# Kernel tuning notes

Hardware: AMD Instinct MI355X
Metric: run time of the kernel (lower is better)

Reference implementation:

```python
import jax, jax.numpy as jnp
import numpy as np

B, T, F = 131072, 15, 12
H1, H2, CS = 64, 128, 96  # num_h1, num_h2, input_feature*8


def _lstm_cell(x, h, c, w_ih, w_hh, b_ih, b_hh):
    # torch.nn.LSTMCell gate order: i, f, g, o
    gates = x @ w_ih.T + h @ w_hh.T + b_ih + b_hh  # [B, 4H]
    i, f, g, o = jnp.split(gates, 4, axis=-1)
    i, f, o = jax.nn.sigmoid(i), jax.nn.sigmoid(f), jax.nn.sigmoid(o)
    g = jnp.tanh(g)
    c_new = f * c + i * g
    h_new = o * jnp.tanh(c_new)
    return h_new, c_new


def setup_inputs() -> dict:
    key = jax.random.key(0)
    ks = jax.random.split(key, 16)
    s = 0.05
    return {
        "input_seq": jax.random.normal(ks[0], (B, T, F), jnp.float32),
        "cell_state": jax.random.normal(ks[1], (B, CS), jnp.float32),
        "fc1_w": jax.random.normal(ks[2], (H1, CS), jnp.float32) * s,
        "fc1_b": jnp.zeros((H1,), jnp.float32),
        "fc2_w": jax.random.normal(ks[3], (H2, CS), jnp.float32) * s,
        "fc2_b": jnp.zeros((H2,), jnp.float32),
        "l0_w_ih": jax.random.normal(ks[4], (4 * H1, F), jnp.float32) * s,
        "l0_w_hh": jax.random.normal(ks[5], (4 * H1, H1), jnp.float32) * s,
        "l0_b_ih": jnp.zeros((4 * H1,), jnp.float32),
        "l0_b_hh": jnp.zeros((4 * H1,), jnp.float32),
        "l1_w_ih": jax.random.normal(ks[6], (4 * H2, H1), jnp.float32) * s,
        "l1_w_hh": jax.random.normal(ks[7], (4 * H2, H2), jnp.float32) * s,
        "l1_b_ih": jnp.zeros((4 * H2,), jnp.float32),
        "l1_b_hh": jnp.zeros((4 * H2,), jnp.float32),
        "d1_w": jax.random.normal(ks[8], (H1, H2), jnp.float32) * s,
        "d1_b": jnp.zeros((H1,), jnp.float32),
        "d2_w": jax.random.normal(ks[9], (1, H1), jnp.float32) * s,
        "d2_b": jnp.zeros((1,), jnp.float32),
    }


def reference(input_seq, cell_state, fc1_w, fc1_b, fc2_w, fc2_b,
              l0_w_ih, l0_w_hh, l0_b_ih, l0_b_hh,
              l1_w_ih, l1_w_hh, l1_b_ih, l1_b_hh,
              d1_w, d1_b, d2_w, d2_b):
    # dropout in eval mode (identity) for deterministic reference
    h0 = jnp.zeros((input_seq.shape[0], H1), input_seq.dtype)
    c0 = cell_state @ fc1_w.T + fc1_b
    h1 = jnp.zeros((input_seq.shape[0], H2), input_seq.dtype)
    c1 = cell_state @ fc2_w.T + fc2_b

    def step(carry, x_t):
        h0, c0, h1, c1 = carry
        h0n, c0_res = _lstm_cell(x_t, h0, c0, l0_w_ih, l0_w_hh, l0_b_ih, l0_b_hh)
        c0n = c0 + c0_res  # residual cell state
        h1n, c1_res = _lstm_cell(h0n, h1, c1, l1_w_ih, l1_w_hh, l1_b_ih, l1_b_hh)
        c1n = c1 + c1_res
        return (h0n, c0n, h1n, c1n), None

    xs = jnp.swapaxes(input_seq, 0, 1)  # [T, B, F]
    (h0, c0, h1, c1), _ = jax.lax.scan(step, (h0, c0, h1, c1), xs)
    pred = (h1 @ d1_w.T + d1_b) @ d2_w.T + d2_b  # [B, 1]
    return pred
```

## Files before the change

### kernel.cpp

```cpp
#include <hip/hip_runtime.h>


typedef float    f32x4 __attribute__((ext_vector_type(4)));
typedef _Float16 f16x8 __attribute__((ext_vector_type(8)));
typedef _Float16 f16x4 __attribute__((ext_vector_type(4)));

#define DEV static __device__ __forceinline__

DEV float fexp2(float x){ return __builtin_amdgcn_exp2f(x); }
DEV float frcp (float x){ return __builtin_amdgcn_rcpf(x); }

#define MFMA16(A,B,C) __builtin_amdgcn_mfma_f32_16x16x32_f16(A,B,C,0,0,0)

constexpr int T = 15, F = 12, CS = 96;
constexpr int R = 64;

constexpr int Q1OFF  = 0;
constexpr int Q0HOFF = 196608;
constexpr int Q0XOFF = 229376;
constexpr int QF2OFF = 245760;
constexpr int QF1OFF = 270336;

constexpr float NL2E = -1.44269504f, PL2E2 = 2.88539008f;

constexpr int OH0 = 0;
constexpr int OH1 = 16384;
constexpr int OX  = 49152;
constexpr int OKC = 57344;
constexpr int OWE = 60416;
constexpr int OWX = 61440;
constexpr int OWH = 77824;
constexpr int OC  = 110592;
constexpr int LDSB= 159744;

__global__ __launch_bounds__(64) void prequant(
    const float* __restrict__ fc1w, const float* __restrict__ fc2w,
    const float* __restrict__ w0i,  const float* __restrict__ w0h,
    const float* __restrict__ w1i,  const float* __restrict__ w1h,
    char* __restrict__ ws)
{
  const int r = blockIdx.x, j = threadIdx.x;
  auto put = [&](long off, float v){ *(_Float16*)(ws + off) = (_Float16)v; };
  if (r < 512){
    int n = r, lr = n & 15, wv = (n & 127) >> 4, g = n >> 7;
    #pragma unroll
    for (int c = 0; c < 3; ++c){
      int k = j + c*64;
      float v = (k < 64) ? w1i[n*64 + k] : w1h[n*128 + (k - 64)];
      int ks = k >> 5, lane = (((k >> 3) & 3) << 4) + lr, jj = k & 7;
      put(Q1OFF + ((long)(((wv*4+g)*6+ks)*64 + lane))*16 + jj*2, v);
    }
  } else if (r < 768){
    int n = r - 512, lr = n & 15, grp = (n & 63) >> 4, g = n >> 6;
    {
      int k = j;
      int ks = k >> 5, lane = (((k >> 3) & 3) << 4) + lr, jj = k & 7;
      put(Q0HOFF + ((long)(((grp*4+g)*2+ks)*64 + lane))*16 + jj*2, w0h[n*64 + k]);
    }
    if (j < 32){
      int k = j;
      int lane = (((k >> 3) & 3) << 4) + lr, jj = k & 7;
      float v = (k < 12) ? w0i[n*12 + k] : 0.f;
      put(Q0XOFF + ((long)((grp*4+g)*64 + lane))*16 + jj*2, v);
    }
  } else {
    bool t2 = (r < 896);
    int n = t2 ? (r - 768) : (r - 896);
    const float* fw = t2 ? fc2w : fc1w;
    long base = t2 ? QF2OFF : QF1OFF;
    int lr = n & 15, grp = n >> 4;
    #pragma unroll
    for (int c = 0; c < 2; ++c){
      int k = j + c*64;
      if (k < 96){
        int ks = k >> 5, lane = (((k >> 3) & 3) << 4) + lr, jj = k & 7;
        put(base + ((long)((grp*3+ks)*64 + lane))*16 + jj*2, fw[n*CS + k]);
      }
    }
  }
}

DEV float cellupd(float t0, float t1, float t2, float t3, float& c){
  float ei = fexp2(t0);
  float ef = fexp2(t1);
  float eg = fexp2(t2);
  float eo = fexp2(t3);
  float e1 = 1.f + ei, e2 = eg + 1.f, e3 = 1.f + ef;
  float m1 = e1 * e2;
  float num = fmaf(c, m1, (eg - 1.f) * e3);
  float tmp = num * frcp(m1 * e3);
  c += tmp;
  float tc = fminf(tmp, 12.0f);
  float ec = fexp2(tc * PL2E2);
  return (ec - 1.f) * frcp((1.f + eo) * (ec + 1.f));
}

__global__ __launch_bounds__(512, 2) void caurec(
    const float* __restrict__ x,    const float* __restrict__ cs,
    const float* __restrict__ fc1b, const float* __restrict__ fc2b,
    const float* __restrict__ b0i,  const float* __restrict__ b0h,
    const float* __restrict__ b1i,  const float* __restrict__ b1h,
    const float* __restrict__ d1w,  const float* __restrict__ d1b,
    const float* __restrict__ d2w,  const float* __restrict__ d2b,
    const char* __restrict__ ws,    float* __restrict__ out)
{
  __shared__ alignas(16) char L[LDSB];

  const int tid  = threadIdx.x;
  const int wave = tid >> 6, lane = tid & 63, lr = lane & 15, lg = lane >> 4;
  const int n0   = (wave & 3) * 16, mB0 = (wave >> 2) * 32, n1 = wave * 16;
  const int grp  = wave & 3;
  const int rowBase = blockIdx.x * R;
  const int sw8  = (lr & 7) << 4;

  const int rb0   = OH0 + lr*128 + ((lg*16) ^ sw8);
  const int rb0w  = rb0 + mB0*128;
  const int rb1   = OH1 + lr*256 + ((lg*16) ^ sw8);
  const int xrdb  = OX + (mB0 + lr)*64 + lg*16;
  const int kadC1 = OKC + wave*256 + lr*16;
  const int kadC0 = OKC + 2048 + grp*256 + lr*16;
  const int cst1  = OH1 + (lg*4)*256 + (((n1 + lr)*2) ^ ((lg & 1) << 6));
  const int cst0  = OH0 + (mB0 + lg*4)*128 + (((n0 + lr)*2) ^ ((lg & 1) << 6));
  const int owxb  = OWX + grp*4096 + lane*16;
  const int owhb  = OWH + grp*8192 + lane*16;
  const int cbase = OC + tid*4;
  const int xr = tid/3, xq = tid - (tid/3)*3;
  const int xst = OX + xr*64 + xq*8;

  {
    unsigned* W = (unsigned*)L;
    for (int i = tid; i < 2048; i += 512) W[2048  + i] = 0u;
    for (int i = tid; i < 4096; i += 512) W[4096  + i] = 0u;
    for (int i = tid; i < 2048; i += 512) W[12288 + i] = 0u;
  }
  __syncthreads();

  {
    int r = tid >> 3, cg = (tid & 7) * 16;
    #pragma unroll
    for (int u = 0; u < 2; ++u){
      f16x8 V;
      #pragma unroll
      for (int q4 = 0; q4 < 2; ++q4){
        int col = cg + u*8 + q4*4;
        float4 v = make_float4(0.f,0.f,0.f,0.f);
        if (col < CS) v = *(const float4*)&cs[(size_t)(rowBase + r)*CS + col];
        V[q4*4+0]=(_Float16)v.x; V[q4*4+1]=(_Float16)v.y;
        V[q4*4+2]=(_Float16)v.z; V[q4*4+3]=(_Float16)v.w;
      }
      int ad = OH1 + 16384 + r*256 + (((cg + u*8)*2) ^ ((r & 7) << 4));
      *(f16x8*)(L + ad) = V;
    }
  }
  if (tid < 192){
    float4 v = *(const float4*)&x[((size_t)(rowBase + xr)*T + 0)*F + xq*4];
    f16x4 w; w[0]=(_Float16)v.x; w[1]=(_Float16)v.y; w[2]=(_Float16)v.z; w[3]=(_Float16)v.w;
    *(f16x4*)(L + xst) = w;
  }
  if (tid < 128){
    float s = 0.f;
    for (int a = 0; a < 64; ++a) s += d2w[a] * d1w[a*128 + tid];
    ((float*)(L + OWE))[tid] = s;
  } else if (tid == 128){
    float s = 0.f;
    for (int a = 0; a < 64; ++a) s += d2w[a] * d1b[a];
    ((float*)(L + OWE))[128] = s + d2b[0];
  }
  if (lg == 0){
    f32x4 c1k, c0k;
    #pragma unroll
    for (int g = 0; g < 4; ++g){
      float f = (g == 2) ? PL2E2 : NL2E;
      c1k[g] = f * (b1i[g*128 + n1 + lr] + b1h[g*128 + n1 + lr]);
      c0k[g] = f * (b0i[g*64  + n0 + lr] + b0h[g*64  + n0 + lr]);
    }
    *(f32x4*)(L + kadC1) = c1k;
    *(f32x4*)(L + kadC0) = c0k;
  }
  #pragma unroll
  for (int k = 0; k < 4; ++k){
    int i = tid + k*512;
    *(long*)(L + OWX + i*8) = *(const long*)(ws + Q0XOFF + i*8);
  }
  #pragma unroll
  for (int k = 0; k < 8; ++k){
    int i = tid + k*512;
    *(long*)(L + OWH + i*8) = *(const long*)(ws + Q0HOFF + i*8);
  }
  f16x8 WB1[4][6];
  #pragma unroll
  for (int g = 0; g < 4; ++g)
    #pragma unroll
    for (int ks = 0; ks < 6; ++ks)
      WB1[g][ks] = *(const f16x8*)(ws + Q1OFF + ((long)(((wave*4+g)*6+ks)*64 + lane))*16);
  __syncthreads();

  {
    const f32x4 Zf = {0.f,0.f,0.f,0.f};
    float bb2 = fc2b[n1 + lr];
    #pragma unroll
    for (int mt = 0; mt < 4; ++mt){
      f32x4 a = Zf;
      #pragma unroll
      for (int ks = 0; ks < 3; ++ks){
        f16x8 A = *(const f16x8*)(L + ((rb1 ^ (ks << 6)) + 16384 + mt*4096));
        f16x8 B = *(const f16x8*)(ws + QF2OFF + ((long)((wave*3+ks)*64 + lane))*16);
        a = MFMA16(A, B, a);
      }
      #pragma unroll
      for (int e = 0; e < 4; ++e)
        *(float*)(L + cbase + (mt*4 + e)*2048) = a[e] + bb2;
    }
    float bb1 = fc1b[n0 + lr];
    #pragma unroll
    for (int mt = 0; mt < 2; ++mt){
      f32x4 a = Zf;
      #pragma unroll
      for (int ks = 0; ks < 3; ++ks){
        f16x8 A = *(const f16x8*)(L + ((rb1 ^ (ks << 6)) + 16384 + mB0*256 + mt*4096));
        f16x8 B = *(const f16x8*)(ws + QF1OFF + ((long)((grp*3+ks)*64 + lane))*16);
        a = MFMA16(A, B, a);
      }
      #pragma unroll
      for (int e = 0; e < 4; ++e)
        *(float*)(L + cbase + ((16 + mt*4) + e)*2048) = a[e] + bb1;
    }
  }
  __syncthreads();

  auto l1_one = [&](int mt, int p8, int p16, int q16){
    const f32x4 Zf = {0.f,0.f,0.f,0.f};
    f32x4 kC = *(const f32x4*)(L + kadC1);
    f16x8 H = *(const f16x8*)(L + (rb0 + p8 + mt*2048));
    f32x4 a0 = MFMA16(H, WB1[0][0], Zf);
    f32x4 a1 = MFMA16(H, WB1[1][0], Zf);
    f32x4 a2 = MFMA16(H, WB1[2][0], Zf);
    f32x4 a3 = MFMA16(H, WB1[3][0], Zf);
    H = *(const f16x8*)(L + ((rb0 ^ 64) + p8 + mt*2048));
    a0 = MFMA16(H, WB1[0][1], a0); a1 = MFMA16(H, WB1[1][1], a1);
    a2 = MFMA16(H, WB1[2][1], a2); a3 = MFMA16(H, WB1[3][1], a3);
    #pragma unroll
    for (int ks = 0; ks < 4; ++ks){
      H = *(const f16x8*)(L + ((rb1 ^ (ks << 6)) + p16 + mt*4096));
      a0 = MFMA16(H, WB1[0][2+ks], a0); a1 = MFMA16(H, WB1[1][2+ks], a1);
      a2 = MFMA16(H, WB1[2][2+ks], a2); a3 = MFMA16(H, WB1[3][2+ks], a3);
    }
    const int sb = cst1 + q16 + mt*4096;
    #pragma unroll
    for (int e = 0; e < 4; ++e){
      float t0 = fmaf(a0[e], NL2E,  kC[0]);
      float t1 = fmaf(a1[e], NL2E,  kC[1]);
      float t2 = fmaf(a2[e], PL2E2, kC[2]);
      float t3 = fmaf(a3[e], NL2E,  kC[3]);
      float cc = *(const float*)(L + cbase + (mt*4 + e)*2048);
      float h = cellupd(t0, t1, t2, t3, cc);
      *(float*)(L + cbase + (mt*4 + e)*2048) = cc;
      *(_Float16*)(L + ((sb + e*256) ^ (e << 4))) = (_Float16)h;
    }
  };

  auto l0_one = [&](int mt, int p8, int px, int q8){
    const f32x4 Zf = {0.f,0.f,0.f,0.f};
    f32x4 kC = *(const f32x4*)(L + kadC0);
    f16x8 X  = *(const f16x8*)(L + (xrdb + px + mt*1024));
    f16x8 H0 = *(const f16x8*)(L + (rb0w + p8 + mt*2048));
    f16x8 H1 = *(const f16x8*)(L + ((rb0w ^ 64) + p8 + mt*2048));
    f32x4 a0, a1, a2, a3;
    {
      f16x8 W0 = *(const f16x8*)(L + owhb + 0*2048);
      f16x8 W1 = *(const f16x8*)(L + owhb + 0*2048 + 1024);
      f16x8 Wx = *(const f16x8*)(L + owxb + 0*1024);
      a0 = MFMA16(H0, W0, Zf); a0 = MFMA16(H1, W1, a0); a0 = MFMA16(X, Wx, a0);
    }
    {
      f16x8 W0 = *(const f16x8*)(L + owhb + 1*2048);
      f16x8 W1 = *(const f16x8*)(L + owhb + 1*2048 + 1024);
      f16x8 Wx = *(const f16x8*)(L + owxb + 1*1024);
      a1 = MFMA16(H0, W0, Zf); a1 = MFMA16(H1, W1, a1); a1 = MFMA16(X, Wx, a1);
    }
    {
      f16x8 W0 = *(const f16x8*)(L + owhb + 2*2048);
      f16x8 W1 = *(const f16x8*)(L + owhb + 2*2048 + 1024);
      f16x8 Wx = *(const f16x8*)(L + owxb + 2*1024);
      a2 = MFMA16(H0, W0, Zf); a2 = MFMA16(H1, W1, a2); a2 = MFMA16(X, Wx, a2);
    }
    {
      f16x8 W0 = *(const f16x8*)(L + owhb + 3*2048);
      f16x8 W1 = *(const f16x8*)(L + owhb + 3*2048 + 1024);
      f16x8 Wx = *(const f16x8*)(L + owxb + 3*1024);
      a3 = MFMA16(H0, W0, Zf); a3 = MFMA16(H1, W1, a3); a3 = MFMA16(X, Wx, a3);
    }
    const int sb = cst0 + q8 + mt*2048;
    #pragma unroll
    for (int e = 0; e < 4; ++e){
      float t0 = fmaf(a0[e], NL2E,  kC[0]);
      float t1 = fmaf(a1[e], NL2E,  kC[1]);
      float t2 = fmaf(a2[e], PL2E2, kC[2]);
      float t3 = fmaf(a3[e], NL2E,  kC[3]);
      float cc = *(const float*)(L + cbase + ((16 + mt*4) + e)*2048);
      float h = cellupd(t0, t1, t2, t3, cc);
      *(float*)(L + cbase + ((16 + mt*4) + e)*2048) = cc;
      *(_Float16*)(L + ((sb + e*128) ^ (e << 4))) = (_Float16)h;
    }
  };

  {
    float4 xv; const bool doX = tid < 192;
    if (doX) xv = *(const float4*)&x[((size_t)(rowBase + xr)*T + 1)*F + xq*4];
    l0_one(0, 8192, 0, 0);
    l0_one(1, 8192, 0, 0);
    if (doX){
      f16x4 w; w[0]=(_Float16)xv.x; w[1]=(_Float16)xv.y; w[2]=(_Float16)xv.z; w[3]=(_Float16)xv.w;
      *(f16x4*)(L + xst + 4096) = w;
    }
    __syncthreads();
  }

  for (int j = 0; j < 7; ++j){
    {
      float4 xv; const bool doX = tid < 192;
      if (doX) xv = *(const float4*)&x[((size_t)(rowBase + xr)*T + (2*j + 2))*F + xq*4];
      l1_one(0, 0, 0, 16384);
      l1_one(1, 0, 0, 16384);
      l0_one(0, 0, 4096, 8192);
      l1_one(2, 0, 0, 16384);
      l0_one(1, 0, 4096, 8192);
      l1_one(3, 0, 0, 16384);
      if (doX){
        f16x4 w; w[0]=(_Float16)xv.x; w[1]=(_Float16)xv.y; w[2]=(_Float16)xv.z; w[3]=(_Float16)xv.w;
        *(f16x4*)(L + xst) = w;
      }
      __syncthreads();
    }
    {
      float4 xv; const bool doX = (j < 6) && (tid < 192);
      if (doX) xv = *(const float4*)&x[((size_t)(rowBase + xr)*T + (2*j + 3))*F + xq*4];
      l1_one(0, 8192, 16384, 0);
      l1_one(1, 8192, 16384, 0);
      l0_one(0, 8192, 0, 0);
      l1_one(2, 8192, 16384, 0);
      l0_one(1, 8192, 0, 0);
      l1_one(3, 8192, 16384, 0);
      if (doX){
        f16x4 w; w[0]=(_Float16)xv.x; w[1]=(_Float16)xv.y; w[2]=(_Float16)xv.z; w[3]=(_Float16)xv.w;
        *(f16x4*)(L + xst + 4096) = w;
      }
      __syncthreads();
    }
  }

  {
    l1_one(0, 0, 0, 16384);
    l1_one(1, 0, 0, 16384);
    l1_one(2, 0, 0, 16384);
    l1_one(3, 0, 0, 16384);
    __syncthreads();
  }

  {
    int r = tid >> 3, s = tid & 7;
    const float* wE = (const float*)(L + OWE);
    float sum = 0.f;
    #pragma unroll
    for (int cc = 0; cc < 16; ++cc){
      int c = s*16 + cc;
      const char* pe = L + OH1 + 16384 + r*256 + ((c*2) ^ ((r & 7) << 4));
      sum += (float)(*(const _Float16*)pe) * wE[c];
    }
    sum += __shfl_down(sum, 4);
    sum += __shfl_down(sum, 2);
    sum += __shfl_down(sum, 1);
    if (s == 0) out[rowBase + r] = sum + wE[128];
  }
}

extern "C" void kernel_launch(void* const* d_in, const int* in_sizes, int n_in,
                              void* d_out, int out_size, void* d_ws, size_t ws_size,
                              hipStream_t stream) {
  const float* x    = (const float*)d_in[0];
  const float* cs   = (const float*)d_in[1];
  const float* fc1w = (const float*)d_in[2];
  const float* fc1b = (const float*)d_in[3];
  const float* fc2w = (const float*)d_in[4];
  const float* fc2b = (const float*)d_in[5];
  const float* w0i  = (const float*)d_in[6];
  const float* w0h  = (const float*)d_in[7];
  const float* b0i  = (const float*)d_in[8];
  const float* b0h  = (const float*)d_in[9];
  const float* w1i  = (const float*)d_in[10];
  const float* w1h  = (const float*)d_in[11];
  const float* b1i  = (const float*)d_in[12];
  const float* b1h  = (const float*)d_in[13];
  const float* d1w  = (const float*)d_in[14];
  const float* d1b  = (const float*)d_in[15];
  const float* d2w  = (const float*)d_in[16];
  const float* d2b  = (const float*)d_in[17];

  char* ws = (char*)d_ws;
  prequant<<<960, 64, 0, stream>>>(fc1w, fc2w, w0i, w0h, w1i, w1h, ws);

  const int Btot = in_sizes[0] / (T * F);
  const int grid = Btot / R;
  caurec<<<grid, 512, 0, stream>>>(x, cs, fc1b, fc2b, b0i, b0h, b1i, b1h,
                                   d1w, d1b, d2w, d2b, ws, (float*)d_out);
}
```

Measured before the change: 645.5 us.

## Keep LSTM cell state, gate biases and layer-0 weights in registers instead of LDS

Moves the per-thread cell state, the scaled gate bias constants and the layer-0 weight fragments out of shared memory and into VGPRs. LDS use per block drops from about 156 KB to about 57 KB, which removes many LDS reads and writes from the recurrent inner loop and may allow two blocks per CU. The cost is higher register pressure, with about 24 extra f16x8 fragments plus 24 floats of cell state per thread, which risks spills or fewer waves.

```diff
diff --git a/kernel.cpp b/kernel.cpp
--- a/kernel.cpp
+++ b/kernel.cpp
@@ -26,12 +26,8 @@
 constexpr int OH0 = 0;
 constexpr int OH1 = 16384;
 constexpr int OX  = 49152;
-constexpr int OKC = 57344;
-constexpr int OWE = 60416;
-constexpr int OWX = 61440;
-constexpr int OWH = 77824;
-constexpr int OC  = 110592;
-constexpr int LDSB= 159744;
+constexpr int OWE = 57344;
+constexpr int LDSB= 58368;
 
 __global__ __launch_bounds__(64) void prequant(
     const float* __restrict__ fc1w, const float* __restrict__ fc2w,
@@ -117,13 +113,8 @@
   const int rb0w  = rb0 + mB0*128;
   const int rb1   = OH1 + lr*256 + ((lg*16) ^ sw8);
   const int xrdb  = OX + (mB0 + lr)*64 + lg*16;
-  const int kadC1 = OKC + wave*256 + lr*16;
-  const int kadC0 = OKC + 2048 + grp*256 + lr*16;
   const int cst1  = OH1 + (lg*4)*256 + (((n1 + lr)*2) ^ ((lg & 1) << 6));
   const int cst0  = OH0 + (mB0 + lg*4)*128 + (((n0 + lr)*2) ^ ((lg & 1) << 6));
-  const int owxb  = OWX + grp*4096 + lane*16;
-  const int owhb  = OWH + grp*8192 + lane*16;
-  const int cbase = OC + tid*4;
   const int xr = tid/3, xq = tid - (tid/3)*3;
   const int xst = OX + xr*64 + xq*8;
 
@@ -166,26 +157,12 @@
     for (int a = 0; a < 64; ++a) s += d2w[a] * d1b[a];
     ((float*)(L + OWE))[128] = s + d2b[0];
   }
-  if (lg == 0){
-    f32x4 c1k, c0k;
-    #pragma unroll
-    for (int g = 0; g < 4; ++g){
-      float f = (g == 2) ? PL2E2 : NL2E;
-      c1k[g] = f * (b1i[g*128 + n1 + lr] + b1h[g*128 + n1 + lr]);
-      c0k[g] = f * (b0i[g*64  + n0 + lr] + b0h[g*64  + n0 + lr]);
-    }
-    *(f32x4*)(L + kadC1) = c1k;
-    *(f32x4*)(L + kadC0) = c0k;
-  }
+  f32x4 kC1v, kC0v;
   #pragma unroll
-  for (int k = 0; k < 4; ++k){
-    int i = tid + k*512;
-    *(long*)(L + OWX + i*8) = *(const long*)(ws + Q0XOFF + i*8);
-  }
-  #pragma unroll
-  for (int k = 0; k < 8; ++k){
-    int i = tid + k*512;
-    *(long*)(L + OWH + i*8) = *(const long*)(ws + Q0HOFF + i*8);
+  for (int g = 0; g < 4; ++g){
+    float f = (g == 2) ? PL2E2 : NL2E;
+    kC1v[g] = f * (b1i[g*128 + n1 + lr] + b1h[g*128 + n1 + lr]);
+    kC0v[g] = f * (b0i[g*64  + n0 + lr] + b0h[g*64  + n0 + lr]);
   }
   f16x8 WB1[4][6];
   #pragma unroll
@@ -193,8 +170,17 @@
     #pragma unroll
     for (int ks = 0; ks < 6; ++ks)
       WB1[g][ks] = *(const f16x8*)(ws + Q1OFF + ((long)(((wave*4+g)*6+ks)*64 + lane))*16);
+  f16x8 WB0h[4][2], WB0x[4];
+  #pragma unroll
+  for (int g = 0; g < 4; ++g){
+    #pragma unroll
+    for (int sp = 0; sp < 2; ++sp)
+      WB0h[g][sp] = *(const f16x8*)(ws + Q0HOFF + ((long)(((grp*4+g)*2+sp)*64 + lane))*16);
+    WB0x[g] = *(const f16x8*)(ws + Q0XOFF + ((long)((grp*4+g)*64 + lane))*16);
+  }
   __syncthreads();
 
+  f32x4 c1r[4], c0r[2];
   {
     const f32x4 Zf = {0.f,0.f,0.f,0.f};
     float bb2 = fc2b[n1 + lr];
@@ -208,8 +194,7 @@
         a = MFMA16(A, B, a);
       }
       #pragma unroll
-      for (int e = 0; e < 4; ++e)
-        *(float*)(L + cbase + (mt*4 + e)*2048) = a[e] + bb2;
+      for (int e = 0; e < 4; ++e) c1r[mt][e] = a[e] + bb2;
     }
     float bb1 = fc1b[n0 + lr];
     #pragma unroll
@@ -222,15 +207,13 @@
         a = MFMA16(A, B, a);
       }
       #pragma unroll
-      for (int e = 0; e < 4; ++e)
-        *(float*)(L + cbase + ((16 + mt*4) + e)*2048) = a[e] + bb1;
+      for (int e = 0; e < 4; ++e) c0r[mt][e] = a[e] + bb1;
     }
   }
   __syncthreads();
 
   auto l1_one = [&](int mt, int p8, int p16, int q16){
     const f32x4 Zf = {0.f,0.f,0.f,0.f};
-    f32x4 kC = *(const f32x4*)(L + kadC1);
     f16x8 H = *(const f16x8*)(L + (rb0 + p8 + mt*2048));
     f32x4 a0 = MFMA16(H, WB1[0][0], Zf);
     f32x4 a1 = MFMA16(H, WB1[1][0], Zf);
@@ -248,58 +231,40 @@
     const int sb = cst1 + q16 + mt*4096;
     #pragma unroll
     for (int e = 0; e < 4; ++e){
-      float t0 = fmaf(a0[e], NL2E,  kC[0]);
-      float t1 = fmaf(a1[e], NL2E,  kC[1]);
-      float t2 = fmaf(a2[e], PL2E2, kC[2]);
-      float t3 = fmaf(a3[e], NL2E,  kC[3]);
-      float cc = *(const float*)(L + cbase + (mt*4 + e)*2048);
+      float t0 = fmaf(a0[e], NL2E,  kC1v[0]);
+      float t1 = fmaf(a1[e], NL2E,  kC1v[1]);
+      float t2 = fmaf(a2[e], PL2E2, kC1v[2]);
+      float t3 = fmaf(a3[e], NL2E,  kC1v[3]);
+      float cc = c1r[mt][e];
       float h = cellupd(t0, t1, t2, t3, cc);
-      *(float*)(L + cbase + (mt*4 + e)*2048) = cc;
+      c1r[mt][e] = cc;
       *(_Float16*)(L + ((sb + e*256) ^ (e << 4))) = (_Float16)h;
     }
   };
 
   auto l0_one = [&](int mt, int p8, int px, int q8){
     const f32x4 Zf = {0.f,0.f,0.f,0.f};
-    f32x4 kC = *(const f32x4*)(L + kadC0);
     f16x8 X  = *(const f16x8*)(L + (xrdb + px + mt*1024));
     f16x8 H0 = *(const f16x8*)(L + (rb0w + p8 + mt*2048));
     f16x8 H1 = *(const f16x8*)(L + ((rb0w ^ 64) + p8 + mt*2048));
-    f32x4 a0, a1, a2, a3;
-    {
-      f16x8 W0 = *(const f16x8*)(L + owhb + 0*2048);
-      f16x8 W1 = *(const f16x8*)(L + owhb + 0*2048 + 1024);
-      f16x8 Wx = *(const f16x8*)(L + owxb + 0*1024);
-      a0 = MFMA16(H0, W0, Zf); a0 = MFMA16(H1, W1, a0); a0 = MFMA16(X, Wx, a0);
-    }
-    {
-      f16x8 W0 = *(const f16x8*)(L + owhb + 1*2048);
-      f16x8 W1 = *(const f16x8*)(L + owhb + 1*2048 + 1024);
-      f16x8 Wx = *(const f16x8*)(L + owxb + 1*1024);
-      a1 = MFMA16(H0, W0, Zf); a1 = MFMA16(H1, W1, a1); a1 = MFMA16(X, Wx, a1);
-    }
-    {
-      f16x8 W0 = *(const f16x8*)(L + owhb + 2*2048);
-      f16x8 W1 = *(const f16x8*)(L + owhb + 2*2048 + 1024);
-      f16x8 Wx = *(const f16x8*)(L + owxb + 2*1024);
-      a2 = MFMA16(H0, W0, Zf); a2 = MFMA16(H1, W1, a2); a2 = MFMA16(X, Wx, a2);
-    }
-    {
-      f16x8 W0 = *(const f16x8*)(L + owhb + 3*2048);
-      f16x8 W1 = *(const f16x8*)(L + owhb + 3*2048 + 1024);
-      f16x8 Wx = *(const f16x8*)(L + owxb + 3*1024);
-      a3 = MFMA16(H0, W0, Zf); a3 = MFMA16(H1, W1, a3); a3 = MFMA16(X, Wx, a3);
-    }
+    f32x4 a0 = MFMA16(H0, WB0h[0][0], Zf);
+    f32x4 a1 = MFMA16(H0, WB0h[1][0], Zf);
+    f32x4 a2 = MFMA16(H0, WB0h[2][0], Zf);
+    f32x4 a3 = MFMA16(H0, WB0h[3][0], Zf);
+    a0 = MFMA16(H1, WB0h[0][1], a0); a1 = MFMA16(H1, WB0h[1][1], a1);
+    a2 = MFMA16(H1, WB0h[2][1], a2); a3 = MFMA16(H1, WB0h[3][1], a3);
+    a0 = MFMA16(X, WB0x[0], a0); a1 = MFMA16(X, WB0x[1], a1);
+    a2 = MFMA16(X, WB0x[2], a2); a3 = MFMA16(X, WB0x[3], a3);
     const int sb = cst0 + q8 + mt*2048;
     #pragma unroll
     for (int e = 0; e < 4; ++e){
-      float t0 = fmaf(a0[e], NL2E,  kC[0]);
-      float t1 = fmaf(a1[e], NL2E,  kC[1]);
-      float t2 = fmaf(a2[e], PL2E2, kC[2]);
-      float t3 = fmaf(a3[e], NL2E,  kC[3]);
-      float cc = *(const float*)(L + cbase + ((16 + mt*4) + e)*2048);
+      float t0 = fmaf(a0[e], NL2E,  kC0v[0]);
+      float t1 = fmaf(a1[e], NL2E,  kC0v[1]);
+      float t2 = fmaf(a2[e], PL2E2, kC0v[2]);
+      float t3 = fmaf(a3[e], NL2E,  kC0v[3]);
+      float cc = c0r[mt][e];
       float h = cellupd(t0, t1, t2, t3, cc);
-      *(float*)(L + cbase + ((16 + mt*4) + e)*2048) = cc;
+      c0r[mt][e] = cc;
       *(_Float16*)(L + ((sb + e*128) ^ (e << 4))) = (_Float16)h;
     }
   };
```

After: 699.4 us. 8.4% more time.
